# Kernel optimization log

Hardware: AMD Instinct MI355X
Metric: run time of the kernel (lower is better)

## Reference

```python
import jax, jax.numpy as jnp
import numpy as np

EPS = 1e-5


def _dwconv(x, w, pad):
    # x: [N,C,H,W]; w: [C,1,k,k] depthwise kernel (groups = C)
    return jax.lax.conv_general_dilated(
        x, w, window_strides=(1, 1), padding=[(pad, pad), (pad, pad)],
        feature_group_count=w.shape[0],
        dimension_numbers=("NCHW", "OIHW", "NCHW"))


def _bn(y, g, b, m, v):
    # inference-mode BatchNorm2d using running stats; per-channel affine
    scale = (g / jnp.sqrt(v + EPS))[None, :, None, None]
    shift = (b - m * g / jnp.sqrt(v + EPS))[None, :, None, None]
    return y * scale + shift


def setup_inputs() -> dict:
    key = jax.random.key(0)
    ks = jax.random.split(key, 16)
    C, KL, KS = 384, 13, 3
    N, H, W = 16, 64, 64
    inp = {
        "x": jax.random.normal(ks[0], (N, C, H, W), jnp.float32),
        "w_large": jax.random.normal(ks[1], (C, 1, KL, KL), jnp.float32) * 0.05,
        "w_small": jax.random.normal(ks[2], (C, 1, KS, KS), jnp.float32) * 0.2,
        "g_l": jax.random.normal(ks[3], (C,), jnp.float32),
        "b_l": jax.random.normal(ks[4], (C,), jnp.float32),
        "m_l": jax.random.normal(ks[5], (C,), jnp.float32),
        "v_l": jax.random.uniform(ks[6], (C,), jnp.float32, 0.5, 1.5),
        "g_s": jax.random.normal(ks[7], (C,), jnp.float32),
        "b_s": jax.random.normal(ks[8], (C,), jnp.float32),
        "m_s": jax.random.normal(ks[9], (C,), jnp.float32),
        "v_s": jax.random.uniform(ks[10], (C,), jnp.float32, 0.5, 1.5),
        "g_i": jax.random.normal(ks[11], (C,), jnp.float32),
        "b_i": jax.random.normal(ks[12], (C,), jnp.float32),
        "m_i": jax.random.normal(ks[13], (C,), jnp.float32),
        "v_i": jax.random.uniform(ks[14], (C,), jnp.float32, 0.5, 1.5),
    }
    return inp


def reference(x, w_large, w_small, g_l, b_l, m_l, v_l,
              g_s, b_s, m_s, v_s, g_i, b_i, m_i, v_i):
    kl = w_large.shape[-1]
    ks = w_small.shape[-1]
    out = (_bn(_dwconv(x, w_large, kl // 2), g_l, b_l, m_l, v_l)
           + _bn(_dwconv(x, w_small, ks // 2), g_s, b_s, m_s, v_s)
           + _bn(x, g_i, b_i, m_i, v_i))
    return out
```

## Files before the change

### kernel.cpp

```cpp
#include <hip/hip_runtime.h>

#define EPSV 1e-5f

typedef __fp16 f16x8 __attribute__((ext_vector_type(8)));
typedef float f32x4 __attribute__((ext_vector_type(4)));
typedef __fp16 half2v __attribute__((ext_vector_type(2)));

__device__ __forceinline__ unsigned h2_as_u32(half2v h) {
    union { half2v h; unsigned u; } cv;
    cv.h = h;
    return cv.u;
}

#define LROWS 76
#define LSTRIDE 88

__global__ __launch_bounds__(256) void fuse_weights(
    const float* __restrict__ w_large, const float* __restrict__ w_small,
    const float* __restrict__ g_l, const float* __restrict__ b_l,
    const float* __restrict__ m_l, const float* __restrict__ v_l,
    const float* __restrict__ g_s, const float* __restrict__ b_s,
    const float* __restrict__ m_s, const float* __restrict__ v_s,
    const float* __restrict__ g_i, const float* __restrict__ b_i,
    const float* __restrict__ m_i, const float* __restrict__ v_i,
    float* __restrict__ bf, uint4* __restrict__ wB) {
    __shared__ float sw[169];
    const int c = blockIdx.x;
    const int t = threadIdx.x;
    const float sl = g_l[c] * rsqrtf(v_l[c] + EPSV);
    const float ss = g_s[c] * rsqrtf(v_s[c] + EPSV);
    const float si = g_i[c] * rsqrtf(v_i[c] + EPSV);
    if (t < 169) {
        const int ky = t / 13, kx = t % 13;
        float w = w_large[c * 169 + t] * sl;
        if (ky >= 5 && ky <= 7 && kx >= 5 && kx <= 7)
            w += w_small[c * 9 + (ky - 5) * 3 + (kx - 5)] * ss;
        if (t == 6 * 13 + 6) w += si;
        sw[t] = w;
    }
    if (t == 0)
        bf[c] = (b_l[c] - m_l[c] * sl) + (b_s[c] - m_s[c] * ss) +
                (b_i[c] - m_i[c] * si);
    __syncthreads();
    for (int it = t; it < 832; it += 256) {
        const int dy = it >> 6;
        const int l = it & 63;
        const int i = l & 15;
        const int kb = (l >> 4) * 8;
        unsigned u[4];
#pragma unroll
        for (int jj = 0; jj < 4; ++jj) {
            const int kx0 = kb + 2 * jj - i - 2;
            const int kx1 = kx0 + 1;
            const float w0 =
                (kx0 >= 0 && kx0 <= 12) ? sw[dy * 13 + kx0] : 0.0f;
            const float w1 =
                (kx1 >= 0 && kx1 <= 12) ? sw[dy * 13 + kx1] : 0.0f;
            u[jj] = h2_as_u32(__builtin_amdgcn_cvt_pkrtz(w0, w1));
        }
        wB[(size_t)c * 832 + it] = make_uint4(u[0], u[1], u[2], u[3]);
    }
}

__global__ __launch_bounds__(256, 4) void dwconv_mfma(
    const float* __restrict__ x, const uint4* __restrict__ wB,
    const float* __restrict__ bf, float* __restrict__ out) {
    __shared__ __align__(16) __fp16 tile[LROWS * LSTRIDE];

    const int t = threadIdx.x;
    const int img = blockIdx.x;
    const int c = __builtin_amdgcn_readfirstlane(img % 384);
    const size_t base = (size_t)img * 4096;

    unsigned* tz = (unsigned*)tile;
    for (int i2 = t; i2 < LROWS * LSTRIDE / 2; i2 += 256) tz[i2] = 0u;
    __syncthreads();

    {
        const int r = t >> 2;
        const int q = t & 3;
        const float* src = x + base + r * 64 + q * 16;
        unsigned u[8];
#pragma unroll
        for (int p = 0; p < 4; ++p) {
            const float4 v = ((const float4*)src)[p];
            u[2 * p + 0] = h2_as_u32(__builtin_amdgcn_cvt_pkrtz(v.x, v.y));
            u[2 * p + 1] = h2_as_u32(__builtin_amdgcn_cvt_pkrtz(v.z, v.w));
        }
        unsigned* dst = tz + (r + 6) * 44 + 4 + q * 8;
        *(uint4*)dst = make_uint4(u[0], u[1], u[2], u[3]);
        *(uint4*)(dst + 4) = make_uint4(u[4], u[5], u[6], u[7]);
    }

    const int l = t & 63;
    const int wv = t >> 6;
    f16x8 Bf[13];
    {
        const uint4* wbp = wB + (size_t)c * 832 + l;
#pragma unroll
        for (int dy = 0; dy < 13; ++dy) {
            union { uint4 u; f16x8 h; } cv;
            cv.u = wbp[dy * 64];
            Bf[dy] = cv.h;
        }
    }
    const float bv = bf[c];
    __syncthreads();

    const int c0 = wv * 16;
    const int lrow = l & 15;
    const int kb = (l >> 4) * 8;
    const __fp16* abase = tile + lrow * LSTRIDE + c0 + kb;

    const int ocol = c0 + (l & 15);
    const int orow = 4 * (l >> 4);

#pragma unroll 1
    for (int rp = 0; rp < 2; ++rp) {
        const int r0a = rp * 32;
        const int r0b = rp * 32 + 16;
        f32x4 accA = {bv, bv, bv, bv};
        f32x4 accB = {bv, bv, bv, bv};
#pragma unroll
        for (int dy = 0; dy < 13; ++dy) {
            const f16x8 a0 = *(const f16x8*)(abase + (r0a + dy) * LSTRIDE);
            const f16x8 a1 = *(const f16x8*)(abase + (r0b + dy) * LSTRIDE);
            accA = __builtin_amdgcn_mfma_f32_16x16x32_f16(a0, Bf[dy], accA,
                                                          0, 0, 0);
            accB = __builtin_amdgcn_mfma_f32_16x16x32_f16(a1, Bf[dy], accB,
                                                          0, 0, 0);
        }
        float* ob = out + base;
#pragma unroll
        for (int q = 0; q < 4; ++q) {
            ob[(r0a + orow + q) * 64 + ocol] = accA[q];
            ob[(r0b + orow + q) * 64 + ocol] = accB[q];
        }
    }
}

extern "C" void kernel_launch(void* const* d_in, const int* in_sizes, int n_in,
                              void* d_out, int out_size, void* d_ws,
                              size_t ws_size, hipStream_t stream) {
    const float* x = (const float*)d_in[0];
    const float* w_large = (const float*)d_in[1];
    const float* w_small = (const float*)d_in[2];
    const float* g_l = (const float*)d_in[3];
    const float* b_l = (const float*)d_in[4];
    const float* m_l = (const float*)d_in[5];
    const float* v_l = (const float*)d_in[6];
    const float* g_s = (const float*)d_in[7];
    const float* b_s = (const float*)d_in[8];
    const float* m_s = (const float*)d_in[9];
    const float* v_s = (const float*)d_in[10];
    const float* g_i = (const float*)d_in[11];
    const float* b_i = (const float*)d_in[12];
    const float* m_i = (const float*)d_in[13];
    const float* v_i = (const float*)d_in[14];
    float* outp = (float*)d_out;

    float* bfp = (float*)d_ws;
    uint4* wB = (uint4*)(bfp + 384);

    fuse_weights<<<384, 256, 0, stream>>>(w_large, w_small, g_l, b_l, m_l, v_l,
                                          g_s, b_s, m_s, v_s, g_i, b_i, m_i,
                                          v_i, bfp, wB);
    dwconv_mfma<<<16 * 384, 256, 0, stream>>>(x, wB, bfp, outp);
}
```

Measured before the change: 41.87 us.

## Zero only halo in LDS, stream weights per row, raise occupancy target

```diff
diff --git a/kernel.cpp b/kernel.cpp
--- a/kernel.cpp
+++ b/kernel.cpp
@@ -62,19 +62,28 @@
     }
 }
 
-__global__ __launch_bounds__(256, 4) void dwconv_mfma(
+__global__ __launch_bounds__(256, 6) void dwconv_mfma(
     const float* __restrict__ x, const uint4* __restrict__ wB,
     const float* __restrict__ bf, float* __restrict__ out) {
     __shared__ __align__(16) __fp16 tile[LROWS * LSTRIDE];
+    unsigned* tz = (unsigned*)tile;
 
     const int t = threadIdx.x;
     const int img = blockIdx.x;
     const int c = __builtin_amdgcn_readfirstlane(img % 384);
     const size_t base = (size_t)img * 4096;
 
-    unsigned* tz = (unsigned*)tile;
-    for (int i2 = t; i2 < LROWS * LSTRIDE / 2; i2 += 256) tz[i2] = 0u;
-    __syncthreads();
+    if (t < 120) {
+        const int r = t / 10;
+        const int rr = (r < 6) ? r : r + 64;
+        const int qq = t - r * 10;
+        *(uint4*)(tz + rr * 44 + qq * 4) = make_uint4(0u, 0u, 0u, 0u);
+    }
+    if (t < 128) {
+        const int r = 6 + (t >> 1);
+        const int sb = (t & 1) ? 36 : 0;
+        *(uint4*)(tz + r * 44 + sb) = make_uint4(0u, 0u, 0u, 0u);
+    }
 
     {
         const int r = t >> 2;
@@ -94,48 +103,48 @@
 
     const int l = t & 63;
     const int wv = t >> 6;
-    f16x8 Bf[13];
-    {
-        const uint4* wbp = wB + (size_t)c * 832 + l;
-#pragma unroll
-        for (int dy = 0; dy < 13; ++dy) {
-            union { uint4 u; f16x8 h; } cv;
-            cv.u = wbp[dy * 64];
-            Bf[dy] = cv.h;
-        }
-    }
-    const float bv = bf[c];
-    __syncthreads();
-
     const int c0 = wv * 16;
     const int lrow = l & 15;
     const int kb = (l >> 4) * 8;
     const __fp16* abase = tile + lrow * LSTRIDE + c0 + kb;
+    const uint4* __restrict__ wbp = wB + (size_t)c * 832 + l;
+    const float bv = bf[c];
+
+    uint4 bcur = wbp[0];
+
+    f32x4 acc0 = {bv, bv, bv, bv};
+    f32x4 acc1 = {bv, bv, bv, bv};
+    f32x4 acc2 = {bv, bv, bv, bv};
+    f32x4 acc3 = {bv, bv, bv, bv};
+
+    __syncthreads();
+
+#pragma unroll 1
+    for (int dy = 0; dy < 13; ++dy) {
+        const int dyn = (dy < 12) ? dy + 1 : 12;
+        const uint4 bnext = wbp[dyn * 64];
+        union { uint4 u; f16x8 h; } bc;
+        bc.u = bcur;
+        const f16x8 a0 = *(const f16x8*)(abase + (dy) * LSTRIDE);
+        const f16x8 a1 = *(const f16x8*)(abase + (16 + dy) * LSTRIDE);
+        const f16x8 a2 = *(const f16x8*)(abase + (32 + dy) * LSTRIDE);
+        const f16x8 a3 = *(const f16x8*)(abase + (48 + dy) * LSTRIDE);
+        acc0 = __builtin_amdgcn_mfma_f32_16x16x32_f16(a0, bc.h, acc0, 0, 0, 0);
+        acc1 = __builtin_amdgcn_mfma_f32_16x16x32_f16(a1, bc.h, acc1, 0, 0, 0);
+        acc2 = __builtin_amdgcn_mfma_f32_16x16x32_f16(a2, bc.h, acc2, 0, 0, 0);
+        acc3 = __builtin_amdgcn_mfma_f32_16x16x32_f16(a3, bc.h, acc3, 0, 0, 0);
+        bcur = bnext;
+    }
 
     const int ocol = c0 + (l & 15);
     const int orow = 4 * (l >> 4);
-
-#pragma unroll 1
-    for (int rp = 0; rp < 2; ++rp) {
-        const int r0a = rp * 32;
-        const int r0b = rp * 32 + 16;
-        f32x4 accA = {bv, bv, bv, bv};
-        f32x4 accB = {bv, bv, bv, bv};
+    float* ob = out + base;
 #pragma unroll
-        for (int dy = 0; dy < 13; ++dy) {
-            const f16x8 a0 = *(const f16x8*)(abase + (r0a + dy) * LSTRIDE);
-            const f16x8 a1 = *(const f16x8*)(abase + (r0b + dy) * LSTRIDE);
-            accA = __builtin_amdgcn_mfma_f32_16x16x32_f16(a0, Bf[dy], accA,
-                                                          0, 0, 0);
-            accB = __builtin_amdgcn_mfma_f32_16x16x32_f16(a1, Bf[dy], accB,
-                                                          0, 0, 0);
-        }
-        float* ob = out + base;
-#pragma unroll
-        for (int q = 0; q < 4; ++q) {
-            ob[(r0a + orow + q) * 64 + ocol] = accA[q];
-            ob[(r0b + orow + q) * 64 + ocol] = accB[q];
-        }
+    for (int q = 0; q < 4; ++q) {
+        ob[(orow + q) * 64 + ocol] = acc0[q];
+        ob[(16 + orow + q) * 64 + ocol] = acc1[q];
+        ob[(32 + orow + q) * 64 + ocol] = acc2[q];
+        ob[(48 + orow + q) * 64 + ocol] = acc3[q];
     }
 }
 
```

Result: slower. 47.21 us (+12.8%).

## Swizzle LDS tile, zero only halos, issue loads early, unroll all four row blocks

Applied to the files above, without the earlier changes.

```diff
diff --git a/kernel.cpp b/kernel.cpp
--- a/kernel.cpp
+++ b/kernel.cpp
@@ -13,7 +13,8 @@
 }
 
 #define LROWS 76
-#define LSTRIDE 88
+#define LSTRH 128
+#define LSTR32 64
 
 __global__ __launch_bounds__(256) void fuse_weights(
     const float* __restrict__ w_large, const float* __restrict__ w_small,
@@ -65,31 +66,50 @@
 __global__ __launch_bounds__(256, 4) void dwconv_mfma(
     const float* __restrict__ x, const uint4* __restrict__ wB,
     const float* __restrict__ bf, float* __restrict__ out) {
-    __shared__ __align__(16) __fp16 tile[LROWS * LSTRIDE];
+    __shared__ __align__(16) unsigned lds[LROWS * LSTR32];
+    __fp16* tile = (__fp16*)lds;
 
     const int t = threadIdx.x;
     const int img = blockIdx.x;
     const int c = __builtin_amdgcn_readfirstlane(img % 384);
     const size_t base = (size_t)img * 4096;
 
-    unsigned* tz = (unsigned*)tile;
-    for (int i2 = t; i2 < LROWS * LSTRIDE / 2; i2 += 256) tz[i2] = 0u;
-    __syncthreads();
+    const int sr = t >> 2;
+    const int sq = t & 3;
+    const float4* srcp = (const float4*)(x + base + sr * 64 + sq * 16);
+    const float4 xr0 = srcp[0];
+    const float4 xr1 = srcp[1];
+    const float4 xr2 = srcp[2];
+    const float4 xr3 = srcp[3];
+
+    if (t < 192) {
+        const int r = t >> 4;
+        const int rr = (r < 6) ? r : r + 64;
+        *(uint4*)(lds + rr * LSTR32 + (t & 15) * 4) =
+            make_uint4(0u, 0u, 0u, 0u);
+    }
+    if (t < 128) {
+        const int r = 6 + (t >> 1);
+        const int lc = (t & 1) ? 9 : 0;
+        const int pc = lc ^ (r & 7);
+        *(uint4*)(lds + r * LSTR32 + pc * 4) = make_uint4(0u, 0u, 0u, 0u);
+    }
 
     {
-        const int r = t >> 2;
-        const int q = t & 3;
-        const float* src = x + base + r * 64 + q * 16;
+        const int R = sr + 6;
         unsigned u[8];
-#pragma unroll
-        for (int p = 0; p < 4; ++p) {
-            const float4 v = ((const float4*)src)[p];
-            u[2 * p + 0] = h2_as_u32(__builtin_amdgcn_cvt_pkrtz(v.x, v.y));
-            u[2 * p + 1] = h2_as_u32(__builtin_amdgcn_cvt_pkrtz(v.z, v.w));
-        }
-        unsigned* dst = tz + (r + 6) * 44 + 4 + q * 8;
-        *(uint4*)dst = make_uint4(u[0], u[1], u[2], u[3]);
-        *(uint4*)(dst + 4) = make_uint4(u[4], u[5], u[6], u[7]);
+        u[0] = h2_as_u32(__builtin_amdgcn_cvt_pkrtz(xr0.x, xr0.y));
+        u[1] = h2_as_u32(__builtin_amdgcn_cvt_pkrtz(xr0.z, xr0.w));
+        u[2] = h2_as_u32(__builtin_amdgcn_cvt_pkrtz(xr1.x, xr1.y));
+        u[3] = h2_as_u32(__builtin_amdgcn_cvt_pkrtz(xr1.z, xr1.w));
+        u[4] = h2_as_u32(__builtin_amdgcn_cvt_pkrtz(xr2.x, xr2.y));
+        u[5] = h2_as_u32(__builtin_amdgcn_cvt_pkrtz(xr2.z, xr2.w));
+        u[6] = h2_as_u32(__builtin_amdgcn_cvt_pkrtz(xr3.x, xr3.y));
+        u[7] = h2_as_u32(__builtin_amdgcn_cvt_pkrtz(xr3.z, xr3.w));
+        const int p0 = (1 + 2 * sq) ^ (R & 7);
+        const int p1 = (2 + 2 * sq) ^ (R & 7);
+        *(uint4*)(lds + R * LSTR32 + p0 * 4) = make_uint4(u[0], u[1], u[2], u[3]);
+        *(uint4*)(lds + R * LSTR32 + p1 * 4) = make_uint4(u[4], u[5], u[6], u[7]);
     }
 
     const int l = t & 63;
@@ -105,37 +125,45 @@
         }
     }
     const float bv = bf[c];
+
     __syncthreads();
 
-    const int c0 = wv * 16;
     const int lrow = l & 15;
-    const int kb = (l >> 4) * 8;
-    const __fp16* abase = tile + lrow * LSTRIDE + c0 + kb;
+    const int cb = 2 * wv + (l >> 4);
+    f32x4 acc0 = {bv, bv, bv, bv};
+    f32x4 acc1 = {bv, bv, bv, bv};
+    f32x4 acc2 = {bv, bv, bv, bv};
+    f32x4 acc3 = {bv, bv, bv, bv};
 
-    const int ocol = c0 + (l & 15);
+#pragma unroll
+    for (int dy = 0; dy < 13; ++dy) {
+        const int Ra = lrow + dy;
+        const int Rb = Ra + 16;
+        const int Rc = Ra + 32;
+        const int Rd = Ra + 48;
+        const f16x8 a0 =
+            *(const f16x8*)(tile + (Ra << 7) + ((cb ^ (Ra & 7)) << 3));
+        const f16x8 a1 =
+            *(const f16x8*)(tile + (Rb << 7) + ((cb ^ (Rb & 7)) << 3));
+        const f16x8 a2 =
+            *(const f16x8*)(tile + (Rc << 7) + ((cb ^ (Rc & 7)) << 3));
+        const f16x8 a3 =
+            *(const f16x8*)(tile + (Rd << 7) + ((cb ^ (Rd & 7)) << 3));
+        acc0 = __builtin_amdgcn_mfma_f32_16x16x32_f16(a0, Bf[dy], acc0, 0, 0, 0);
+        acc1 = __builtin_amdgcn_mfma_f32_16x16x32_f16(a1, Bf[dy], acc1, 0, 0, 0);
+        acc2 = __builtin_amdgcn_mfma_f32_16x16x32_f16(a2, Bf[dy], acc2, 0, 0, 0);
+        acc3 = __builtin_amdgcn_mfma_f32_16x16x32_f16(a3, Bf[dy], acc3, 0, 0, 0);
+    }
+
+    const int ocol = 16 * wv + (l & 15);
     const int orow = 4 * (l >> 4);
-
-#pragma unroll 1
-    for (int rp = 0; rp < 2; ++rp) {
-        const int r0a = rp * 32;
-        const int r0b = rp * 32 + 16;
-        f32x4 accA = {bv, bv, bv, bv};
-        f32x4 accB = {bv, bv, bv, bv};
+    float* ob = out + base;
 #pragma unroll
-        for (int dy = 0; dy < 13; ++dy) {
-            const f16x8 a0 = *(const f16x8*)(abase + (r0a + dy) * LSTRIDE);
-            const f16x8 a1 = *(const f16x8*)(abase + (r0b + dy) * LSTRIDE);
-            accA = __builtin_amdgcn_mfma_f32_16x16x32_f16(a0, Bf[dy], accA,
-                                                          0, 0, 0);
-            accB = __builtin_amdgcn_mfma_f32_16x16x32_f16(a1, Bf[dy], accB,
-                                                          0, 0, 0);
-        }
-        float* ob = out + base;
-#pragma unroll
-        for (int q = 0; q < 4; ++q) {
-            ob[(r0a + orow + q) * 64 + ocol] = accA[q];
-            ob[(r0b + orow + q) * 64 + ocol] = accB[q];
-        }
+    for (int q = 0; q < 4; ++q) {
+        ob[(orow + q) * 64 + ocol] = acc0[q];
+        ob[(16 + orow + q) * 64 + ocol] = acc1[q];
+        ob[(32 + orow + q) * 64 + ocol] = acc2[q];
+        ob[(48 + orow + q) * 64 + ocol] = acc3[q];
     }
 }
 
```

Result: no change. 41.98 us (+0.2%).

## Use 512-thread blocks, zero only LDS halo, issue global loads before zeroing

Applied to the files above, without the earlier changes.

```diff
diff --git a/kernel.cpp b/kernel.cpp
--- a/kernel.cpp
+++ b/kernel.cpp
@@ -13,7 +13,8 @@
 }
 
 #define LROWS 76
-#define LSTRIDE 88
+#define LSTRH 88
+#define LSTR32 44
 
 __global__ __launch_bounds__(256) void fuse_weights(
     const float* __restrict__ w_large, const float* __restrict__ w_small,
@@ -62,38 +63,50 @@
     }
 }
 
-__global__ __launch_bounds__(256, 4) void dwconv_mfma(
+__global__ __launch_bounds__(512, 6) void dwconv_mfma(
     const float* __restrict__ x, const uint4* __restrict__ wB,
     const float* __restrict__ bf, float* __restrict__ out) {
-    __shared__ __align__(16) __fp16 tile[LROWS * LSTRIDE];
+    __shared__ __align__(16) unsigned lds[LROWS * LSTR32];
+    __fp16* tile = (__fp16*)lds;
 
     const int t = threadIdx.x;
     const int img = blockIdx.x;
     const int c = __builtin_amdgcn_readfirstlane(img % 384);
     const size_t base = (size_t)img * 4096;
 
-    unsigned* tz = (unsigned*)tile;
-    for (int i2 = t; i2 < LROWS * LSTRIDE / 2; i2 += 256) tz[i2] = 0u;
-    __syncthreads();
+    const int sr = t >> 3;
+    const int sq = t & 7;
+    const float4* srcp = (const float4*)(x + base + sr * 64 + sq * 8);
+    const float4 xa = srcp[0];
+    const float4 xb = srcp[1];
+
+    if (t < 132) {
+        const int r = t / 11;
+        const int rr = (r < 6) ? r : r + 64;
+        const int qq = t - r * 11;
+        *(uint4*)(lds + rr * LSTR32 + qq * 4) = make_uint4(0u, 0u, 0u, 0u);
+    }
+    if (t >= 320) {
+        const int i = t - 320;
+        const int r = 6 + i / 3;
+        const int s = i % 3;
+        const int sb = (s == 0) ? 0 : (s == 1 ? 36 : 40);
+        *(uint4*)(lds + r * LSTR32 + sb) = make_uint4(0u, 0u, 0u, 0u);
+    }
 
     {
-        const int r = t >> 2;
-        const int q = t & 3;
-        const float* src = x + base + r * 64 + q * 16;
-        unsigned u[8];
-#pragma unroll
-        for (int p = 0; p < 4; ++p) {
-            const float4 v = ((const float4*)src)[p];
-            u[2 * p + 0] = h2_as_u32(__builtin_amdgcn_cvt_pkrtz(v.x, v.y));
-            u[2 * p + 1] = h2_as_u32(__builtin_amdgcn_cvt_pkrtz(v.z, v.w));
-        }
-        unsigned* dst = tz + (r + 6) * 44 + 4 + q * 8;
-        *(uint4*)dst = make_uint4(u[0], u[1], u[2], u[3]);
-        *(uint4*)(dst + 4) = make_uint4(u[4], u[5], u[6], u[7]);
+        const int R = sr + 6;
+        unsigned u0 = h2_as_u32(__builtin_amdgcn_cvt_pkrtz(xa.x, xa.y));
+        unsigned u1 = h2_as_u32(__builtin_amdgcn_cvt_pkrtz(xa.z, xa.w));
+        unsigned u2 = h2_as_u32(__builtin_amdgcn_cvt_pkrtz(xb.x, xb.y));
+        unsigned u3 = h2_as_u32(__builtin_amdgcn_cvt_pkrtz(xb.z, xb.w));
+        *(uint4*)(lds + R * LSTR32 + 4 + sq * 4) = make_uint4(u0, u1, u2, u3);
     }
 
     const int l = t & 63;
     const int wv = t >> 6;
+    const int ct = wv & 3;
+    const int rh = wv >> 2;
     f16x8 Bf[13];
     {
         const uint4* wbp = wB + (size_t)c * 832 + l;
@@ -105,37 +118,31 @@
         }
     }
     const float bv = bf[c];
+
     __syncthreads();
 
-    const int c0 = wv * 16;
     const int lrow = l & 15;
     const int kb = (l >> 4) * 8;
-    const __fp16* abase = tile + lrow * LSTRIDE + c0 + kb;
+    const __fp16* abase = tile + (32 * rh + lrow) * LSTRH + 16 * ct + kb;
 
-    const int ocol = c0 + (l & 15);
-    const int orow = 4 * (l >> 4);
+    f32x4 acc0 = {bv, bv, bv, bv};
+    f32x4 acc1 = {bv, bv, bv, bv};
 
-#pragma unroll 1
-    for (int rp = 0; rp < 2; ++rp) {
-        const int r0a = rp * 32;
-        const int r0b = rp * 32 + 16;
-        f32x4 accA = {bv, bv, bv, bv};
-        f32x4 accB = {bv, bv, bv, bv};
 #pragma unroll
-        for (int dy = 0; dy < 13; ++dy) {
-            const f16x8 a0 = *(const f16x8*)(abase + (r0a + dy) * LSTRIDE);
-            const f16x8 a1 = *(const f16x8*)(abase + (r0b + dy) * LSTRIDE);
-            accA = __builtin_amdgcn_mfma_f32_16x16x32_f16(a0, Bf[dy], accA,
-                                                          0, 0, 0);
-            accB = __builtin_amdgcn_mfma_f32_16x16x32_f16(a1, Bf[dy], accB,
-                                                          0, 0, 0);
-        }
-        float* ob = out + base;
+    for (int dy = 0; dy < 13; ++dy) {
+        const f16x8 a0 = *(const f16x8*)(abase + (dy) * LSTRH);
+        const f16x8 a1 = *(const f16x8*)(abase + (16 + dy) * LSTRH);
+        acc0 = __builtin_amdgcn_mfma_f32_16x16x32_f16(a0, Bf[dy], acc0, 0, 0, 0);
+        acc1 = __builtin_amdgcn_mfma_f32_16x16x32_f16(a1, Bf[dy], acc1, 0, 0, 0);
+    }
+
+    const int ocol = 16 * ct + (l & 15);
+    const int orow = 32 * rh + 4 * (l >> 4);
+    float* ob = out + base;
 #pragma unroll
-        for (int q = 0; q < 4; ++q) {
-            ob[(r0a + orow + q) * 64 + ocol] = accA[q];
-            ob[(r0b + orow + q) * 64 + ocol] = accB[q];
-        }
+    for (int q = 0; q < 4; ++q) {
+        ob[(orow + q) * 64 + ocol] = acc0[q];
+        ob[(orow + 16 + q) * 64 + ocol] = acc1[q];
     }
 }
 
@@ -165,5 +172,5 @@
     fuse_weights<<<384, 256, 0, stream>>>(w_large, w_small, g_l, b_l, m_l, v_l,
                                           g_s, b_s, m_s, v_s, g_i, b_i, m_i,
                                           v_i, bfp, wB);
-    dwconv_mfma<<<16 * 384, 256, 0, stream>>>(x, wB, bfp, outp);
+    dwconv_mfma<<<16 * 384, 512, 0, stream>>>(x, wB, bfp, outp);
 }
```

After: 45.79 us. 1.09x slower.
